# Performance work log

Measured on AMD Instinct MI355X. Metric: run time of the kernel, lower is better.

Reference implementation:

```python
import jax, jax.numpy as jnp
import numpy as np

PENALTY_FACTOR = 2.0
THRESHOLD = 0.01


def setup_inputs() -> dict:
    key = jax.random.key(0)
    k1, k2 = jax.random.split(key)
    B, N = 256, 65536
    prediction = jax.random.normal(k1, (B, N), dtype=jnp.float32)
    label = jax.random.normal(k2, (B, N), dtype=jnp.float32)
    return {"prediction": prediction, "label": label}


def _first_last_significant(mask, half):
    # mask: [B, half] bool. Returns per-row first/last True index,
    # defaulting to (0, half-1) when the row has no True entries
    # (matching the torch fallback branch).
    any_m = jnp.any(mask, axis=1)
    first = jnp.argmax(mask, axis=1)                      # 0 if all False
    last = (half - 1) - jnp.argmax(mask[:, ::-1], axis=1)  # half-1 if all False
    first = jnp.where(any_m, first, 0)
    last = jnp.where(any_m, last, half - 1)
    return first, last


def reference(prediction, label):
    B, N = label.shape
    half = N // 2
    label_real, label_imag = label[:, :half], label[:, half:]
    pred_real, pred_imag = prediction[:, :half], prediction[:, half:]

    label_phase = jnp.arctan2(label_imag, label_real)
    pred_phase = jnp.arctan2(pred_imag, pred_real)
    label_int = label_real ** 2 + label_imag ** 2
    pred_int = pred_real ** 2 + pred_imag ** 2

    fr, lr = _first_last_significant(jnp.abs(label_real) > THRESHOLD, half)
    fi, li = _first_last_significant(jnp.abs(label_imag) > THRESHOLD, half)

    idx = jnp.arange(half)[None, :]  # [1, half]
    w_real = jnp.where((idx < fr[:, None]) | (idx > lr[:, None]), PENALTY_FACTOR, 1.0)
    w_imag = jnp.where((idx < fi[:, None]) | (idx > li[:, None]), PENALTY_FACTOR, 1.0)

    mse_real = w_real * (pred_real - label_real) ** 2
    mse_imag = w_imag * (pred_imag - label_imag) ** 2
    mse_int = (pred_int - label_int) ** 2
    mse_phase = (pred_phase - label_phase) ** 2

    per_sample = (mse_real.mean(axis=1) + mse_imag.mean(axis=1)
                  + 50.0 * mse_int.mean(axis=1) + 0.0 * mse_phase.mean(axis=1))
    return per_sample.mean()
```

## Files before the change

### kernel.cpp

```cpp
#include <hip/hip_runtime.h>
#include <climits>

constexpr int HALF = 32768;
constexpr int TPB  = 256;
constexpr int NSEG = HALF / 4 / TPB;
constexpr float THRESH = 0.01f;

__global__ __launch_bounds__(TPB)
void main_kernel(const float* __restrict__ pred, const float* __restrict__ label,
                 float* __restrict__ part_sum, int4* __restrict__ part_idx)
{
    const int seg = blockIdx.x, row = blockIdx.y;
    const int t = threadIdx.x, wave = t >> 6, lane = t & 63;

    const size_t rb4 = (size_t)row * (size_t)(2 * HALF / 4);
    const int v = seg * TPB + t;
    const float4* lr4 = (const float4*)label + rb4;
    const float4* pr4 = (const float4*)pred + rb4;

    float4 a  = lr4[v];
    float4 b  = lr4[v + HALF / 4];
    float4 pp = pr4[v];
    float4 q  = pr4[v + HALF / 4];

    const int base = v * 4;
    float sum = 0.f;
    int minr = INT_MAX, maxr = -1, mini = INT_MAX, maxi = -1;

#define STEP(ax, bx, px, qx, idx)                                 \
    {                                                             \
        float dr = (px) - (ax), di = (qx) - (bx);                 \
        float lint = (ax) * (ax) + (bx) * (bx);                   \
        float pint = (px) * (px) + (qx) * (qx);                   \
        float dd = pint - lint;                                   \
        sum += dr * dr + di * di + 50.f * dd * dd;                \
        if (fabsf(ax) > THRESH) {                                 \
            minr = min(minr, (idx)); maxr = max(maxr, (idx));     \
        }                                                         \
        if (fabsf(bx) > THRESH) {                                 \
            mini = min(mini, (idx)); maxi = max(maxi, (idx));     \
        }                                                         \
    }
    STEP(a.x, b.x, pp.x, q.x, base + 0)
    STEP(a.y, b.y, pp.y, q.y, base + 1)
    STEP(a.z, b.z, pp.z, q.z, base + 2)
    STEP(a.w, b.w, pp.w, q.w, base + 3)
#undef STEP

    #pragma unroll
    for (int off = 32; off > 0; off >>= 1) {
        sum += __shfl_down(sum, off);
        minr = min(minr, __shfl_down(minr, off));
        maxr = max(maxr, __shfl_down(maxr, off));
        mini = min(mini, __shfl_down(mini, off));
        maxi = max(maxi, __shfl_down(maxi, off));
    }

    __shared__ float s_sum[4];
    __shared__ int   s_idx[4][4];
    if (lane == 0) {
        s_sum[wave] = sum;
        s_idx[wave][0] = minr; s_idx[wave][1] = maxr;
        s_idx[wave][2] = mini; s_idx[wave][3] = maxi;
    }
    __syncthreads();
    if (t == 0) {
        float S = 0.f; int mr = INT_MAX, Mr = -1, mi = INT_MAX, Mi = -1;
        #pragma unroll
        for (int w = 0; w < 4; ++w) {
            S += s_sum[w];
            mr = min(mr, s_idx[w][0]); Mr = max(Mr, s_idx[w][1]);
            mi = min(mi, s_idx[w][2]); Mi = max(Mi, s_idx[w][3]);
        }
        const int slot = seg * gridDim.y + row;
        part_sum[slot] = S;
        part_idx[slot] = make_int4(mr, Mr, mi, Mi);
    }
}

__global__ __launch_bounds__(TPB)
void tail_kernel(const float* __restrict__ pred, const float* __restrict__ label,
                 const float* __restrict__ part_sum, const int4* __restrict__ part_idx,
                 float* __restrict__ out, int rows)
{
    const int t = threadIdx.x, wave = t >> 6, lane = t & 63;

    float total = 0.f;
    if (t < rows) {
        float S = 0.f;
        int fr = INT_MAX, lastr = -1, fi = INT_MAX, lasti = -1;
        for (int s = 0; s < NSEG; ++s) {
            const int slot = s * rows + t;
            S += part_sum[slot];
            int4 v = part_idx[slot];
            fr = min(fr, v.x); lastr = max(lastr, v.y);
            fi = min(fi, v.z); lasti = max(lasti, v.w);
        }
        if (lastr < 0) { fr = 0; lastr = HALF - 1; }
        if (lasti < 0) { fi = 0; lasti = HALF - 1; }

        const float* Lr = label + (size_t)t * (2 * HALF);
        const float* Li = Lr + HALF;
        const float* Pr = pred + (size_t)t * (2 * HALF);
        const float* Pi = Pr + HALF;

        for (int i = 0; i < fr; ++i)            { float d = Pr[i] - Lr[i]; S += d * d; }
        for (int i = lastr + 1; i < HALF; ++i)  { float d = Pr[i] - Lr[i]; S += d * d; }
        for (int i = 0; i < fi; ++i)            { float d = Pi[i] - Li[i]; S += d * d; }
        for (int i = lasti + 1; i < HALF; ++i)  { float d = Pi[i] - Li[i]; S += d * d; }

        total = S;
    }

    #pragma unroll
    for (int off = 32; off > 0; off >>= 1) total += __shfl_down(total, off);
    __shared__ float s[4];
    if (lane == 0) s[wave] = total;
    __syncthreads();
    if (t == 0)
        out[0] = (s[0] + s[1] + s[2] + s[3]) * (1.0f / ((float)HALF * (float)rows));
}

extern "C" void kernel_launch(void* const* d_in, const int* in_sizes, int n_in,
                              void* d_out, int out_size, void* d_ws, size_t ws_size,
                              hipStream_t stream) {
    const float* pred  = (const float*)d_in[0];
    const float* label = (const float*)d_in[1];
    float* out = (float*)d_out;

    const int rows = in_sizes[0] / (2 * HALF);
    const int nslots = rows * NSEG;

    float* part_sum = (float*)d_ws;
    int4*  part_idx = (int4*)((char*)d_ws + nslots * 4);

    dim3 gridA(NSEG, rows);
    main_kernel<<<gridA, TPB, 0, stream>>>(pred, label, part_sum, part_idx);
    tail_kernel<<<1, TPB, 0, stream>>>(pred, label, part_sum, part_idx, out, rows);
}
```

Before: 29.48 us.

## Parallelize edge penalty pass per row and process two vectors per thread

The single-block tail kernel, where one thread serially walked each row's edge regions and summed all partials, is replaced by a per-row edge kernel that spreads that work across a whole block, followed by a tiny finalize kernel. The main kernel now handles two float4 groups per thread, which halves the number of blocks and partial slots, and the partials are stored row-major so each row reads contiguous data. This is meant to remove the serial tail latency. In exchange it adds an extra kernel launch and needs more workspace for the per-row totals.

```diff
diff --git a/kernel.cpp b/kernel.cpp
--- a/kernel.cpp
+++ b/kernel.cpp
@@ -1,29 +1,32 @@
 #include <hip/hip_runtime.h>
 #include <climits>
 
-constexpr int HALF = 32768;
-constexpr int TPB  = 256;
-constexpr int NSEG = HALF / 4 / TPB;
+constexpr int HALF  = 32768;
+constexpr int TPB   = 256;
+constexpr int CHUNK = 2048;
+constexpr int NCHNK = HALF / CHUNK;
 constexpr float THRESH = 0.01f;
 
 __global__ __launch_bounds__(TPB)
 void main_kernel(const float* __restrict__ pred, const float* __restrict__ label,
                  float* __restrict__ part_sum, int4* __restrict__ part_idx)
 {
-    const int seg = blockIdx.x, row = blockIdx.y;
+    const int chunk = blockIdx.x, row = blockIdx.y;
     const int t = threadIdx.x, wave = t >> 6, lane = t & 63;
 
     const size_t rb4 = (size_t)row * (size_t)(2 * HALF / 4);
-    const int v = seg * TPB + t;
     const float4* lr4 = (const float4*)label + rb4;
     const float4* pr4 = (const float4*)pred + rb4;
 
-    float4 a  = lr4[v];
-    float4 b  = lr4[v + HALF / 4];
-    float4 pp = pr4[v];
-    float4 q  = pr4[v + HALF / 4];
+    const int v0 = chunk * (CHUNK / 4) + t;
+    const int v1 = v0 + TPB;
+    const int H4 = HALF / 4;
 
-    const int base = v * 4;
+    float4 a0 = lr4[v0],      a1 = lr4[v1];
+    float4 b0 = lr4[v0 + H4], b1 = lr4[v1 + H4];
+    float4 p0 = pr4[v0],      p1 = pr4[v1];
+    float4 q0 = pr4[v0 + H4], q1 = pr4[v1 + H4];
+
     float sum = 0.f;
     int minr = INT_MAX, maxr = -1, mini = INT_MAX, maxi = -1;
 
@@ -41,10 +44,20 @@
             mini = min(mini, (idx)); maxi = max(maxi, (idx));     \
         }                                                         \
     }
-    STEP(a.x, b.x, pp.x, q.x, base + 0)
-    STEP(a.y, b.y, pp.y, q.y, base + 1)
-    STEP(a.z, b.z, pp.z, q.z, base + 2)
-    STEP(a.w, b.w, pp.w, q.w, base + 3)
+    {
+        const int base = v0 * 4;
+        STEP(a0.x, b0.x, p0.x, q0.x, base + 0)
+        STEP(a0.y, b0.y, p0.y, q0.y, base + 1)
+        STEP(a0.z, b0.z, p0.z, q0.z, base + 2)
+        STEP(a0.w, b0.w, p0.w, q0.w, base + 3)
+    }
+    {
+        const int base = v1 * 4;
+        STEP(a1.x, b1.x, p1.x, q1.x, base + 0)
+        STEP(a1.y, b1.y, p1.y, q1.y, base + 1)
+        STEP(a1.z, b1.z, p1.z, q1.z, base + 2)
+        STEP(a1.w, b1.w, p1.w, q1.w, base + 3)
+    }
 #undef STEP
 
     #pragma unroll
@@ -72,50 +85,62 @@
             mr = min(mr, s_idx[w][0]); Mr = max(Mr, s_idx[w][1]);
             mi = min(mi, s_idx[w][2]); Mi = max(Mi, s_idx[w][3]);
         }
-        const int slot = seg * gridDim.y + row;
+        const int slot = row * NCHNK + chunk;
         part_sum[slot] = S;
         part_idx[slot] = make_int4(mr, Mr, mi, Mi);
     }
 }
 
 __global__ __launch_bounds__(TPB)
-void tail_kernel(const float* __restrict__ pred, const float* __restrict__ label,
+void edge_kernel(const float* __restrict__ pred, const float* __restrict__ label,
                  const float* __restrict__ part_sum, const int4* __restrict__ part_idx,
-                 float* __restrict__ out, int rows)
+                 float* __restrict__ row_tot)
 {
+    const int row = blockIdx.x;
     const int t = threadIdx.x, wave = t >> 6, lane = t & 63;
 
-    float total = 0.f;
-    if (t < rows) {
-        float S = 0.f;
-        int fr = INT_MAX, lastr = -1, fi = INT_MAX, lasti = -1;
-        for (int s = 0; s < NSEG; ++s) {
-            const int slot = s * rows + t;
-            S += part_sum[slot];
-            int4 v = part_idx[slot];
-            fr = min(fr, v.x); lastr = max(lastr, v.y);
-            fi = min(fi, v.z); lasti = max(lasti, v.w);
-        }
-        if (lastr < 0) { fr = 0; lastr = HALF - 1; }
-        if (lasti < 0) { fi = 0; lasti = HALF - 1; }
+    float base = 0.f;
+    int fr = INT_MAX, lastr = -1, fi = INT_MAX, lasti = -1;
+    #pragma unroll
+    for (int s = 0; s < NCHNK; ++s) {
+        base += part_sum[row * NCHNK + s];
+        int4 v = part_idx[row * NCHNK + s];
+        fr = min(fr, v.x); lastr = max(lastr, v.y);
+        fi = min(fi, v.z); lasti = max(lasti, v.w);
+    }
+    if (lastr < 0) { fr = 0; lastr = HALF - 1; }
+    if (lasti < 0) { fi = 0; lasti = HALF - 1; }
 
-        const float* Lr = label + (size_t)t * (2 * HALF);
-        const float* Li = Lr + HALF;
-        const float* Pr = pred + (size_t)t * (2 * HALF);
-        const float* Pi = Pr + HALF;
+    const float* Lr = label + (size_t)row * (2 * HALF);
+    const float* Li = Lr + HALF;
+    const float* Pr = pred + (size_t)row * (2 * HALF);
+    const float* Pi = Pr + HALF;
 
-        for (int i = 0; i < fr; ++i)            { float d = Pr[i] - Lr[i]; S += d * d; }
-        for (int i = lastr + 1; i < HALF; ++i)  { float d = Pr[i] - Lr[i]; S += d * d; }
-        for (int i = 0; i < fi; ++i)            { float d = Pi[i] - Li[i]; S += d * d; }
-        for (int i = lasti + 1; i < HALF; ++i)  { float d = Pi[i] - Li[i]; S += d * d; }
-
-        total = S;
-    }
+    float ex = 0.f;
+    for (int i = t; i < fr; i += TPB)               { float d = Pr[i] - Lr[i]; ex += d * d; }
+    for (int i = lastr + 1 + t; i < HALF; i += TPB) { float d = Pr[i] - Lr[i]; ex += d * d; }
+    for (int i = t; i < fi; i += TPB)               { float d = Pi[i] - Li[i]; ex += d * d; }
+    for (int i = lasti + 1 + t; i < HALF; i += TPB) { float d = Pi[i] - Li[i]; ex += d * d; }
 
     #pragma unroll
-    for (int off = 32; off > 0; off >>= 1) total += __shfl_down(total, off);
+    for (int off = 32; off > 0; off >>= 1) ex += __shfl_down(ex, off);
+    __shared__ float s_ex[4];
+    if (lane == 0) s_ex[wave] = ex;
+    __syncthreads();
+    if (t == 0)
+        row_tot[row] = base + s_ex[0] + s_ex[1] + s_ex[2] + s_ex[3];
+}
+
+__global__ void finalize_kernel(const float* __restrict__ row_tot,
+                                float* __restrict__ out, int rows)
+{
+    const int t = threadIdx.x;
+    float v = 0.f;
+    for (int i = t; i < rows; i += 256) v += row_tot[i];
+    #pragma unroll
+    for (int off = 32; off > 0; off >>= 1) v += __shfl_down(v, off);
     __shared__ float s[4];
-    if (lane == 0) s[wave] = total;
+    if ((t & 63) == 0) s[t >> 6] = v;
     __syncthreads();
     if (t == 0)
         out[0] = (s[0] + s[1] + s[2] + s[3]) * (1.0f / ((float)HALF * (float)rows));
@@ -129,12 +154,14 @@
     float* out = (float*)d_out;
 
     const int rows = in_sizes[0] / (2 * HALF);
-    const int nslots = rows * NSEG;
+    const int nslots = rows * NCHNK;
 
     float* part_sum = (float*)d_ws;
     int4*  part_idx = (int4*)((char*)d_ws + nslots * 4);
+    float* row_tot  = (float*)((char*)d_ws + nslots * 4 + nslots * 16);
 
-    dim3 gridA(NSEG, rows);
+    dim3 gridA(NCHNK, rows);
     main_kernel<<<gridA, TPB, 0, stream>>>(pred, label, part_sum, part_idx);
-    tail_kernel<<<1, TPB, 0, stream>>>(pred, label, part_sum, part_idx, out, rows);
+    edge_kernel<<<rows, TPB, 0, stream>>>(pred, label, part_sum, part_idx, row_tot);
+    finalize_kernel<<<1, 256, 0, stream>>>(row_tot, out, rows);
 }
```

After: 29.29 us. Within noise of the previous version (-0.7%).
